# Performance work log

Measured on AMD Instinct MI355X. Metric: run time of the kernel, lower is better.

## Reference

```python
import jax, jax.numpy as jnp
import numpy as np

N_ORDER = 256
PRED_LEN = 192
SEQ_LEN = 768
ENC_IN = 21
BATCH = 16
MULTISCALE = [1, 2, 4]
MODES = 32  # min(32, min(pred_len, seq_len)//2)


def _transition(N):
    Q = np.arange(N, dtype=np.float64)
    R = (2 * Q + 1)[:, None]
    j, i = np.meshgrid(Q, Q)
    A = np.where(i < j, -1, (-1.0) ** (i - j + 1)) * R
    B = (-1.0) ** Q[:, None] * R
    return A, B


def _bilinear(A, B, dt):
    # scipy cont2discrete(method='bilinear'): Ad=(I-dt/2 A)^-1 (I+dt/2 A), Bd=(I-dt/2 A)^-1 dt B
    N = A.shape[0]
    I = np.eye(N)
    ima = I - (dt / 2.0) * A
    Ad = np.linalg.solve(ima, I + (dt / 2.0) * A)
    Bd = np.linalg.solve(ima, dt * B)
    return Ad, Bd.squeeze(-1)


def _legendre_eval(N, x):
    # Legendre P_n(x) via three-term recurrence; returns [len(x), N]
    T = x.shape[0]
    P = np.zeros((N, T))
    P[0] = 1.0
    if N > 1:
        P[1] = x
    for n in range(2, N):
        P[n] = ((2 * n - 1) * x * P[n - 1] - (n - 1) * P[n - 2]) / n
    return P.T


def setup_inputs() -> dict:
    key = jax.random.key(0)
    ks = jax.random.split(key, 12)
    inp = {"x_enc": jax.random.normal(ks[0], (BATCH, SEQ_LEN, ENC_IN), dtype=jnp.float32)}
    Ac, Bc = _transition(N_ORDER)
    scale = 1.0 / (N_ORDER * N_ORDER)
    for idx, m in enumerate(MULTISCALE):
        dt = 1.0 / PRED_LEN / m
        Ad, Bd = _bilinear(Ac, Bc, dt)
        vals = np.arange(0.0, 1.0, dt)
        E = _legendre_eval(N_ORDER, 1.0 - 2.0 * vals)
        inp[f"A{idx}"] = jnp.asarray(Ad, jnp.float32)
        inp[f"B{idx}"] = jnp.asarray(Bd, jnp.float32)
        inp[f"E{idx}"] = jnp.asarray(E, jnp.float32)
        inp[f"Wr{idx}"] = scale * jax.random.uniform(ks[1 + 2 * idx], (N_ORDER, N_ORDER, MODES), dtype=jnp.float32)
        inp[f"Wi{idx}"] = scale * jax.random.uniform(ks[2 + 2 * idx], (N_ORDER, N_ORDER, MODES), dtype=jnp.float32)
    inp["mlp_w"] = 0.1 * jax.random.normal(ks[10], (1, len(MULTISCALE)), dtype=jnp.float32)
    inp["mlp_b"] = jnp.zeros((1,), jnp.float32)
    return inp


def _hippo(x, A, Bv):
    # x: [B, E, L]; c_t = c_{t-1} @ A^T + f_t * B  (F.linear(c, A) == c @ A.T)
    def step(c, f):
        c = c @ A.T + f[..., None] * Bv
        return c, c
    c0 = jnp.zeros(x.shape[:-1] + (A.shape[0],), x.dtype)
    _, cs = jax.lax.scan(step, c0, jnp.moveaxis(x, -1, 0))
    return jnp.moveaxis(cs, 0, -1)  # [B, E, N, L]


def _spec_conv(x, Wr, Wi):
    # x: [B, E, N_in, L]; keep first MODES rfft modes, complex channel mix, irfft
    L = x.shape[-1]
    a = jnp.fft.rfft(x, axis=-1)[..., :MODES]
    W = (Wr + 1j * Wi).astype(jnp.complex64)
    out = jnp.einsum('bjix,iox->bjox', a, W)
    nf = L // 2 + 1
    out_full = jnp.pad(out, ((0, 0), (0, 0), (0, 0), (0, nf - MODES)))
    return jnp.fft.irfft(out_full, n=L, axis=-1)


def reference(x_enc, A0, B0, E0, Wr0, Wi0, A1, B1, E1, Wr1, Wi1, A2, B2, E2, Wr2, Wi2, mlp_w, mlp_b):
    params = [(A0, B0, E0, Wr0, Wi0), (A1, B1, E1, Wr1, Wi1), (A2, B2, E2, Wr2, Wi2)]
    x_decs = []
    for m, (A, Bv, E, Wr, Wi) in zip(MULTISCALE, params):
        x_in = x_enc[:, -m * PRED_LEN:]                      # [B, L, E]
        c = _hippo(jnp.transpose(x_in, (0, 2, 1)), A, Bv)    # [B, E, N, L]
        out1 = _spec_conv(c, Wr, Wi)                         # [B, E, N, L]
        x_dec_c = out1[:, :, :, PRED_LEN - 1]                # seq_len >= pred_len, jump_dist=0
        x_decs.append(x_dec_c @ E[-PRED_LEN:].T)             # [B, E, pred_len]
    x_dec = jnp.stack(x_decs, axis=-1)                       # [B, E, pred_len, 3]
    out = x_dec @ mlp_w[0] + mlp_b[0]                        # Linear(3,1) then squeeze
    return jnp.transpose(out, (0, 2, 1))                     # [B, pred_len, E]
```

## Files before the change

kernel.cpp:

```cpp
#include <hip/hip_runtime.h>
#include <math.h>

#define PI_F 3.14159265358979323846f

#define W_OFF    0
#define AP_OFF   344064
#define KT_OFF   737280
#define KTOT_OFF 995328
#define Y_OFF    1142784
#define S_OFF    1142784
#define F_OFF    1732608
#define QT_OFF   10579968
#define WS_FLOATS 27095040

__device__ __forceinline__ int off_w_f(int s)  { return 49152  * ((1 << s) - 1); }
__device__ __forceinline__ int qoff_f(int s)   { return 2359296 * ((1 << s) - 1); }
__device__ __forceinline__ int ktoff_f(int s)  { return 36864  * ((1 << s) - 1); }
__device__ __forceinline__ int foff_f(int s)   { return 1179648 * ((1 << s) - 1); }

template<bool BT>
__device__ __forceinline__ void gemm_tile(const float* __restrict__ A,
                                          const float* __restrict__ B,
                                          float* __restrict__ C,
                                          int M, int N, int ldc, int m0, int n0)
{
    __shared__ float As[16][68];
    __shared__ float Bs[16][68];
    const int tid = threadIdx.x;
    const int tx = tid & 15;
    const int ty = tid >> 4;
    const int r  = tid >> 2;
    const int kq = (tid & 3) << 2;

    float acc[4][4] = {{0.f,0.f,0.f,0.f},{0.f,0.f,0.f,0.f},
                       {0.f,0.f,0.f,0.f},{0.f,0.f,0.f,0.f}};

    for (int kk = 0; kk < 256; kk += 16) {
        float4 av = make_float4(0.f, 0.f, 0.f, 0.f);
        if (m0 + r < M)
            av = *(const float4*)(A + (size_t)(m0 + r) * 256 + kk + kq);
        As[kq + 0][r] = av.x; As[kq + 1][r] = av.y;
        As[kq + 2][r] = av.z; As[kq + 3][r] = av.w;

        if (BT) {
            float4 bv = make_float4(0.f, 0.f, 0.f, 0.f);
            if (n0 + r < N)
                bv = *(const float4*)(B + (size_t)(n0 + r) * 256 + kk + kq);
            Bs[kq + 0][r] = bv.x; Bs[kq + 1][r] = bv.y;
            Bs[kq + 2][r] = bv.z; Bs[kq + 3][r] = bv.w;
        } else {
            const int kb = tid >> 4;
            const int j4 = (tid & 15) << 2;
            float4 bv = *(const float4*)(B + (size_t)(kk + kb) * 256 + n0 + j4);
            *(float4*)(&Bs[kb][j4]) = bv;
        }
        __syncthreads();

        #pragma unroll
        for (int k = 0; k < 16; ++k) {
            float4 a4 = *(const float4*)(&As[k][ty << 2]);
            float4 b4 = *(const float4*)(&Bs[k][tx << 2]);
            acc[0][0] = fmaf(a4.x, b4.x, acc[0][0]);
            acc[0][1] = fmaf(a4.x, b4.y, acc[0][1]);
            acc[0][2] = fmaf(a4.x, b4.z, acc[0][2]);
            acc[0][3] = fmaf(a4.x, b4.w, acc[0][3]);
            acc[1][0] = fmaf(a4.y, b4.x, acc[1][0]);
            acc[1][1] = fmaf(a4.y, b4.y, acc[1][1]);
            acc[1][2] = fmaf(a4.y, b4.z, acc[1][2]);
            acc[1][3] = fmaf(a4.y, b4.w, acc[1][3]);
            acc[2][0] = fmaf(a4.z, b4.x, acc[2][0]);
            acc[2][1] = fmaf(a4.z, b4.y, acc[2][1]);
            acc[2][2] = fmaf(a4.z, b4.z, acc[2][2]);
            acc[2][3] = fmaf(a4.z, b4.w, acc[2][3]);
            acc[3][0] = fmaf(a4.w, b4.x, acc[3][0]);
            acc[3][1] = fmaf(a4.w, b4.y, acc[3][1]);
            acc[3][2] = fmaf(a4.w, b4.z, acc[3][2]);
            acc[3][3] = fmaf(a4.w, b4.w, acc[3][3]);
        }
        __syncthreads();
    }

    #pragma unroll
    for (int u = 0; u < 4; ++u) {
        int row = m0 + (ty << 2) + u;
        if (row < M) {
            float4 cv = make_float4(acc[u][0], acc[u][1], acc[u][2], acc[u][3]);
            *(float4*)(C + (size_t)row * ldc + n0 + (tx << 2)) = cv;
        }
    }
}

__device__ __forceinline__ void gemm64x128(const float* __restrict__ A,
                                           const float* __restrict__ B,
                                           float* __restrict__ C, int ldc)
{
    __shared__ float As[16][68];
    __shared__ float Bs[16][132];

    const int tid = threadIdx.x;
    const int tx = tid & 15;
    const int ty = tid >> 4;
    const int ra  = tid >> 2;
    const int kqa = (tid & 3) << 2;
    const int rb  = tid >> 1;
    const int kq8 = (tid & 1) << 3;

    float acc[2][4][4];
    #pragma unroll
    for (int g = 0; g < 2; ++g)
        #pragma unroll
        for (int u = 0; u < 4; ++u)
            #pragma unroll
            for (int v = 0; v < 4; ++v) acc[g][u][v] = 0.f;

    for (int kk = 0; kk < 256; kk += 16) {
        float4 av = *(const float4*)(A + (size_t)ra * 256 + kk + kqa);
        As[kqa + 0][ra] = av.x; As[kqa + 1][ra] = av.y;
        As[kqa + 2][ra] = av.z; As[kqa + 3][ra] = av.w;

        const float* bp = B + (size_t)rb * 256 + kk + kq8;
        float4 b0 = *(const float4*)(bp);
        float4 b1 = *(const float4*)(bp + 4);
        Bs[kq8 + 0][rb] = b0.x; Bs[kq8 + 1][rb] = b0.y;
        Bs[kq8 + 2][rb] = b0.z; Bs[kq8 + 3][rb] = b0.w;
        Bs[kq8 + 4][rb] = b1.x; Bs[kq8 + 5][rb] = b1.y;
        Bs[kq8 + 6][rb] = b1.z; Bs[kq8 + 7][rb] = b1.w;
        __syncthreads();

        #pragma unroll
        for (int kq = 0; kq < 16; ++kq) {
            float4 a  = *(const float4*)(&As[kq][4 * ty]);
            float4 b0v = *(const float4*)(&Bs[kq][4 * tx]);
            float4 b1v = *(const float4*)(&Bs[kq][4 * tx + 64]);
            float af[4] = {a.x, a.y, a.z, a.w};
            float bf[8] = {b0v.x, b0v.y, b0v.z, b0v.w, b1v.x, b1v.y, b1v.z, b1v.w};
            #pragma unroll
            for (int g = 0; g < 2; ++g)
                #pragma unroll
                for (int u = 0; u < 4; ++u)
                    #pragma unroll
                    for (int v = 0; v < 4; ++v)
                        acc[g][u][v] = fmaf(af[u], bf[g * 4 + v], acc[g][u][v]);
        }
        __syncthreads();
    }

    #pragma unroll
    for (int u = 0; u < 4; ++u) {
        int row = 4 * ty + u;
        #pragma unroll
        for (int g = 0; g < 2; ++g) {
            float4 cv = make_float4(acc[g][u][0], acc[g][u][1],
                                    acc[g][u][2], acc[g][u][3]);
            *(float4*)(C + (size_t)row * ldc + 4 * tx + 64 * g) = cv;
        }
    }
}

__global__ void k_init(const float* B0, const float* B1, const float* B2, float* ws)
{
    int s = blockIdx.x;
    const float* Bv = (s == 0) ? B0 : (s == 1) ? B1 : B2;
    ws[W_OFF + off_w_f(s) + threadIdx.x] = Bv[threadIdx.x];
}

__global__ void k_level(int n, const float* A0, const float* A1, const float* A2,
                        float* ws)
{
    int s = blockIdx.z;
    int L = 192 << s;
    const float* Ain = (s == 0) ? A0 : (s == 1) ? A1 : A2;
    float* wbase = ws + W_OFF + off_w_f(s);
    float* bufA  = ws + AP_OFF + s * 131072;
    float* bufB  = bufA + 65536;
    const float* src = (n == 0) ? Ain : (((n - 1) & 1) ? bufB : bufA);

    int y = blockIdx.y;
    if (y < 4) {
        int p2 = 1 << n;
        if (p2 >= L) return;
        int cnt = min(p2, L - p2);
        int m0 = y * 64;
        if (m0 >= cnt) return;
        gemm_tile<true>(wbase, src, wbase + (size_t)p2 * 256,
                        cnt, 256, 256, m0, blockIdx.x * 64);
    } else {
        if ((2 << n) >= L) return;
        float* dst = (n & 1) ? bufB : bufA;
        gemm_tile<false>(src, src, dst, 256, 256, 256, (y - 4) * 64, blockIdx.x * 64);
    }
}

__global__ void k_transpose(const float* Wr0, const float* Wi0,
                            const float* Wr1, const float* Wi1,
                            const float* Wr2, const float* Wi2, float* ws)
{
    int bid = blockIdx.x;
    int i  = bid & 255;
    int ri = (bid >> 8) & 1;
    int s  = bid >> 9;
    const float* W;
    if (s == 0)      W = ri ? Wi0 : Wr0;
    else if (s == 1) W = ri ? Wi1 : Wr1;
    else             W = ri ? Wi2 : Wr2;

    int o = threadIdx.x;
    int sri = s * 2 + ri;
    const float* Wrow = W + (size_t)i * 8192 + (size_t)o * 32;
    #pragma unroll
    for (int k = 0; k < 32; ++k) {
        ws[QT_OFF + ((size_t)(sri * 32 + k) * 256 + i) * 256 + o] = Wrow[k];
    }
}

__global__ void __launch_bounds__(256, 4)
k_gemm_Y4(const float* E0, const float* E1, const float* E2, float* __restrict__ ws)
{
    const int s  = blockIdx.z;
    const int L  = 192 << s;
    const int zz = blockIdx.x >> 1;
    const int n0 = (blockIdx.x & 1) * 128;
    const int z  = s * 64 + zz;
    const int m0 = blockIdx.y * 64;
    const float* E = (s == 0) ? E0 : (s == 1) ? E1 : E2;

    const float* Ap = E + (size_t)(L - 192) * 256 + (size_t)m0 * 256;
    const float* Bp = ws + QT_OFF + (size_t)z * 65536 + (size_t)n0 * 256;
    float* Cp = ws + Y_OFF + (size_t)z * 49152 + (size_t)m0 * 256 + n0;
    gemm64x128(Ap, Bp, Cp, 256);
}

__global__ void __launch_bounds__(256, 4)
k_gemm_Q4(float* __restrict__ ws)
{
    const int y = blockIdx.y;
    int s, yt;
    if (y < 3)      { s = 0; yt = y; }
    else if (y < 9) { s = 1; yt = y - 3; }
    else            { s = 2; yt = y - 9; }
    const int m0 = yt * 64;
    const int n0 = blockIdx.x * 128;

    const float* Ap = ws + W_OFF + off_w_f(s) + (size_t)m0 * 256;
    const float* Bp = ws + Y_OFF + (size_t)s * 3145728 + (size_t)n0 * 256;
    float* Cp = ws + QT_OFF + qoff_f(s) + (size_t)m0 * 12288 + n0;
    gemm64x128(Ap, Bp, Cp, 12288);
}

__global__ void k_scanA(float* __restrict__ ws)
{
    const int c = blockIdx.x;
    const int k = blockIdx.y;
    const int s = blockIdx.z;
    const int L = 192 << s;
    const int C = L >> 4;
    const int p = threadIdx.x;

    __shared__ float twc[768], tws[768];
    for (int m = p; m < L; m += 192) {
        float ang = -2.f * PI_F * (float)m / (float)L;
        float ss, cc; sincosf(ang, &ss, &cc);
        twc[m] = cc; tws[m] = ss;
    }
    __syncthreads();

    const float* Qr = ws + QT_OFF + qoff_f(s) + (size_t)k * 192;
    const float* Qi = Qr + 6144;

    float ar = 0.f, ai = 0.f;
    const int d0 = c * C;
    int ph = (k * d0) % L;
    for (int j = 0; j < C; ++j) {
        int d = d0 + j;
        float qr = Qr[(size_t)d * 12288 + p];
        float qi = Qi[(size_t)d * 12288 + p];
        float cc = twc[ph], sn = tws[ph];
        ar = fmaf(cc, qr, fmaf(-sn, qi, ar));
        ai = fmaf(cc, qi, fmaf( sn, qr, ai));
        ph += k; if (ph >= L) ph -= L;
    }
    size_t sb = (size_t)((s * 32 + k) * 16 + c) * 384;
    ws[S_OFF + sb + p]       = ar;
    ws[S_OFF + sb + 192 + p] = ai;
}

__global__ void k_scanB(float* __restrict__ ws)
{
    const int c = blockIdx.x;
    const int k = blockIdx.y;
    const int s = blockIdx.z;
    const int L = 192 << s;
    const int C = L >> 4;
    const int p = threadIdx.x;

    __shared__ float twc[768], tws[768];
    for (int m = p; m < L; m += 192) {
        float ang = -2.f * PI_F * (float)m / (float)L;
        float ss, cc; sincosf(ang, &ss, &cc);
        twc[m] = cc; tws[m] = ss;
    }
    __syncthreads();

    float ar = 0.f, ai = 0.f;
    size_t sbase = (size_t)(s * 32 + k) * 16 * 384;
    for (int c2 = 0; c2 < c; ++c2) {
        ar += ws[S_OFF + sbase + (size_t)c2 * 384 + p];
        ai += ws[S_OFF + sbase + (size_t)c2 * 384 + 192 + p];
    }

    const float ck = ((k == 0) ? 1.f : 2.f) / (float)L;
    const float* Qr = ws + QT_OFF + qoff_f(s) + (size_t)k * 192;
    const float* Qi = Qr + 6144;
    float* F = ws + F_OFF + foff_f(s);

    const int d0 = c * C;
    int ph = (k * d0) % L;
    int m1 = d0 + 192 - L; if (m1 < 0) m1 += L;
    int ph2 = (k * m1) % L;
    for (int j = 0; j < C; ++j) {
        int d = d0 + j;
        float qr = Qr[(size_t)d * 12288 + p];
        float qi = Qi[(size_t)d * 12288 + p];
        float cc = twc[ph], sn = tws[ph];
        ar = fmaf(cc, qr, fmaf(-sn, qi, ar));
        ai = fmaf(cc, qi, fmaf( sn, qr, ai));
        float f = ck * fmaf(twc[ph2], ar, tws[ph2] * ai);
        int sidx = L - 1 - d;
        F[((size_t)sidx * 32 + k) * 192 + p] = f;
        ph  += k; if (ph  >= L) ph  -= L;
        ph2 += k; if (ph2 >= L) ph2 -= L;
    }
}

__global__ void k_kred(float* __restrict__ ws)
{
    int bid = blockIdx.x;
    int s, sidx;
    if (bid < 192)      { s = 0; sidx = bid; }
    else if (bid < 576) { s = 1; sidx = bid - 192; }
    else                { s = 2; sidx = bid - 576; }
    int p = threadIdx.x;
    const float* F = ws + F_OFF + foff_f(s) + (size_t)sidx * 32 * 192;
    float sum = 0.f;
    #pragma unroll
    for (int k = 0; k < 32; ++k)
        sum += F[k * 192 + p];
    ws[KT_OFF + ktoff_f(s) + (size_t)sidx * 192 + p] = sum;
}

__global__ void k_combine(float* ws, const float* mw)
{
    int idx = blockIdx.x * 256 + threadIdx.x;
    if (idx >= 147456) return;
    int tau = idx / 192;
    int p   = idx - tau * 192;
    float sum = 0.f;
    #pragma unroll
    for (int s = 0; s < 3; ++s) {
        int L = 192 << s;
        int off = 768 - L;
        if (tau >= off)
            sum = fmaf(mw[s], ws[KT_OFF + ktoff_f(s) + (size_t)(tau - off) * 192 + p], sum);
    }
    ws[KTOT_OFF + idx] = sum;
}

__global__ void k_out(const float* __restrict__ x, const float* __restrict__ ws,
                      const float* __restrict__ mb, float* __restrict__ out)
{
    int bid = blockIdx.x;
    int b = bid / 21;
    int c = bid - b * 21;
    __shared__ float xl[768];
    for (int t = threadIdx.x; t < 768; t += 192)
        xl[t] = x[((size_t)b * 768 + t) * 21 + c];
    __syncthreads();

    int p = threadIdx.x;
    const float* K = ws + KTOT_OFF;
    float acc = 0.f;
    for (int tau = 0; tau < 768; ++tau)
        acc = fmaf(xl[tau], K[(size_t)tau * 192 + p], acc);
    out[((size_t)b * 192 + p) * 21 + c] = acc + mb[0];
}

extern "C" void kernel_launch(void* const* d_in, const int* in_sizes, int n_in,
                              void* d_out, int out_size, void* d_ws, size_t ws_size,
                              hipStream_t stream)
{
    const float* x   = (const float*)d_in[0];
    const float* A0  = (const float*)d_in[1];
    const float* B0  = (const float*)d_in[2];
    const float* E0  = (const float*)d_in[3];
    const float* Wr0 = (const float*)d_in[4];
    const float* Wi0 = (const float*)d_in[5];
    const float* A1  = (const float*)d_in[6];
    const float* B1  = (const float*)d_in[7];
    const float* E1  = (const float*)d_in[8];
    const float* Wr1 = (const float*)d_in[9];
    const float* Wi1 = (const float*)d_in[10];
    const float* A2  = (const float*)d_in[11];
    const float* B2  = (const float*)d_in[12];
    const float* E2  = (const float*)d_in[13];
    const float* Wr2 = (const float*)d_in[14];
    const float* Wi2 = (const float*)d_in[15];
    const float* mw  = (const float*)d_in[16];
    const float* mb  = (const float*)d_in[17];
    float* ws  = (float*)d_ws;
    float* out = (float*)d_out;

    if (ws_size < (size_t)WS_FLOATS * sizeof(float)) {
        hipMemsetAsync(d_out, 0, (size_t)out_size * sizeof(float), stream);
        return;
    }

    k_init<<<3, 256, 0, stream>>>(B0, B1, B2, ws);
    for (int n = 0; n < 10; ++n)
        k_level<<<dim3(4, 8, 3), 256, 0, stream>>>(n, A0, A1, A2, ws);
    k_transpose<<<1536, 256, 0, stream>>>(Wr0, Wi0, Wr1, Wi1, Wr2, Wi2, ws);
    k_gemm_Y4<<<dim3(128, 3, 3), 256, 0, stream>>>(E0, E1, E2, ws);
    k_gemm_Q4<<<dim3(96, 21), 256, 0, stream>>>(ws);
    k_scanA<<<dim3(16, 32, 3), 192, 0, stream>>>(ws);
    k_scanB<<<dim3(16, 32, 3), 192, 0, stream>>>(ws);
    k_kred<<<1344, 192, 0, stream>>>(ws);
    k_combine<<<576, 256, 0, stream>>>(ws, mw);
    k_out<<<336, 192, 0, stream>>>(x, ws, mb, out);
}
```

Measured before the change: 471.4 us.

## Coalesce weight transpose via LDS, fuse k-reduction with combine, trim level launches

```diff
diff --git a/kernel.cpp b/kernel.cpp
--- a/kernel.cpp
+++ b/kernel.cpp
@@ -15,7 +15,6 @@
 
 __device__ __forceinline__ int off_w_f(int s)  { return 49152  * ((1 << s) - 1); }
 __device__ __forceinline__ int qoff_f(int s)   { return 2359296 * ((1 << s) - 1); }
-__device__ __forceinline__ int ktoff_f(int s)  { return 36864  * ((1 << s) - 1); }
 __device__ __forceinline__ int foff_f(int s)   { return 1179648 * ((1 << s) - 1); }
 
 template<bool BT>
@@ -90,9 +89,9 @@
     }
 }
 
-__device__ __forceinline__ void gemm64x128(const float* __restrict__ A,
-                                           const float* __restrict__ B,
-                                           float* __restrict__ C, int ldc)
+__device__ __forceinline__ void gemm64x128_q(const float* __restrict__ A,
+                                             const float* __restrict__ B,
+                                             float* __restrict__ C, int ldc)
 {
     __shared__ float As[16][68];
     __shared__ float Bs[16][132];
@@ -129,7 +128,7 @@
 
         #pragma unroll
         for (int kq = 0; kq < 16; ++kq) {
-            float4 a  = *(const float4*)(&As[kq][4 * ty]);
+            float4 a   = *(const float4*)(&As[kq][4 * ty]);
             float4 b0v = *(const float4*)(&Bs[kq][4 * tx]);
             float4 b1v = *(const float4*)(&Bs[kq][4 * tx + 64]);
             float af[4] = {a.x, a.y, a.z, a.w};
@@ -164,10 +163,10 @@
     ws[W_OFF + off_w_f(s) + threadIdx.x] = Bv[threadIdx.x];
 }
 
-__global__ void k_level(int n, const float* A0, const float* A1, const float* A2,
-                        float* ws)
-{
-    int s = blockIdx.z;
+__global__ void k_level(int n, int sbase, const float* A0, const float* A1,
+                        const float* A2, float* ws)
+{
+    int s = blockIdx.z + sbase;
     int L = 192 << s;
     const float* Ain = (s == 0) ? A0 : (s == 1) ? A1 : A2;
     float* wbase = ws + W_OFF + off_w_f(s);
@@ -195,6 +194,7 @@
                             const float* Wr1, const float* Wi1,
                             const float* Wr2, const float* Wi2, float* ws)
 {
+    __shared__ float t[256][33];
     int bid = blockIdx.x;
     int i  = bid & 255;
     int ri = (bid >> 8) & 1;
@@ -204,30 +204,40 @@
     else if (s == 1) W = ri ? Wi1 : Wr1;
     else             W = ri ? Wi2 : Wr2;
 
-    int o = threadIdx.x;
+    const int tid = threadIdx.x;
+    const float* slab = W + (size_t)i * 8192;
+    #pragma unroll
+    for (int j = 0; j < 8; ++j) {
+        int f = j * 1024 + tid * 4;
+        float4 v = *(const float4*)(slab + f);
+        int o = f >> 5;
+        int k = f & 31;
+        t[o][k + 0] = v.x; t[o][k + 1] = v.y;
+        t[o][k + 2] = v.z; t[o][k + 3] = v.w;
+    }
+    __syncthreads();
+
     int sri = s * 2 + ri;
-    const float* Wrow = W + (size_t)i * 8192 + (size_t)o * 32;
     #pragma unroll
     for (int k = 0; k < 32; ++k) {
-        ws[QT_OFF + ((size_t)(sri * 32 + k) * 256 + i) * 256 + o] = Wrow[k];
+        ws[QT_OFF + (size_t)(sri * 32 + k) * 65536 + (size_t)i * 256 + tid] = t[tid][k];
     }
 }
 
 __global__ void __launch_bounds__(256, 4)
-k_gemm_Y4(const float* E0, const float* E1, const float* E2, float* __restrict__ ws)
-{
-    const int s  = blockIdx.z;
+k_gemm_Y5(const float* E0, const float* E1, const float* E2, float* __restrict__ ws)
+{
+    const int z  = blockIdx.z;
+    const int s  = z >> 6;
     const int L  = 192 << s;
-    const int zz = blockIdx.x >> 1;
-    const int n0 = (blockIdx.x & 1) * 128;
-    const int z  = s * 64 + zz;
+    const int n0 = blockIdx.x * 128;
     const int m0 = blockIdx.y * 64;
     const float* E = (s == 0) ? E0 : (s == 1) ? E1 : E2;
 
     const float* Ap = E + (size_t)(L - 192) * 256 + (size_t)m0 * 256;
     const float* Bp = ws + QT_OFF + (size_t)z * 65536 + (size_t)n0 * 256;
     float* Cp = ws + Y_OFF + (size_t)z * 49152 + (size_t)m0 * 256 + n0;
-    gemm64x128(Ap, Bp, Cp, 256);
+    gemm64x128_q(Ap, Bp, Cp, 256);
 }
 
 __global__ void __launch_bounds__(256, 4)
@@ -244,7 +254,7 @@
     const float* Ap = ws + W_OFF + off_w_f(s) + (size_t)m0 * 256;
     const float* Bp = ws + Y_OFF + (size_t)s * 3145728 + (size_t)n0 * 256;
     float* Cp = ws + QT_OFF + qoff_f(s) + (size_t)m0 * 12288 + n0;
-    gemm64x128(Ap, Bp, Cp, 12288);
+    gemm64x128_q(Ap, Bp, Cp, 12288);
 }
 
 __global__ void k_scanA(float* __restrict__ ws)
@@ -332,37 +342,26 @@
     }
 }
 
-__global__ void k_kred(float* __restrict__ ws)
-{
-    int bid = blockIdx.x;
-    int s, sidx;
-    if (bid < 192)      { s = 0; sidx = bid; }
-    else if (bid < 576) { s = 1; sidx = bid - 192; }
-    else                { s = 2; sidx = bid - 576; }
-    int p = threadIdx.x;
-    const float* F = ws + F_OFF + foff_f(s) + (size_t)sidx * 32 * 192;
-    float sum = 0.f;
-    #pragma unroll
-    for (int k = 0; k < 32; ++k)
-        sum += F[k * 192 + p];
-    ws[KT_OFF + ktoff_f(s) + (size_t)sidx * 192 + p] = sum;
-}
-
-__global__ void k_combine(float* ws, const float* mw)
-{
-    int idx = blockIdx.x * 256 + threadIdx.x;
-    if (idx >= 147456) return;
-    int tau = idx / 192;
-    int p   = idx - tau * 192;
+__global__ void k_kredc(float* __restrict__ ws, const float* __restrict__ mw)
+{
+    const int tau = blockIdx.x;
+    const int p   = threadIdx.x;
     float sum = 0.f;
     #pragma unroll
     for (int s = 0; s < 3; ++s) {
         int L = 192 << s;
         int off = 768 - L;
-        if (tau >= off)
-            sum = fmaf(mw[s], ws[KT_OFF + ktoff_f(s) + (size_t)(tau - off) * 192 + p], sum);
-    }
-    ws[KTOT_OFF + idx] = sum;
+        if (tau >= off) {
+            int sidx = tau - off;
+            const float* F = ws + F_OFF + foff_f(s) + (size_t)sidx * 32 * 192;
+            float kt = 0.f;
+            #pragma unroll
+            for (int k = 0; k < 32; ++k)
+                kt += F[k * 192 + p];
+            sum = fmaf(mw[s], kt, sum);
+        }
+    }
+    ws[KTOT_OFF + (size_t)tau * 192 + p] = sum;
 }
 
 __global__ void k_out(const float* __restrict__ x, const float* __restrict__ ws,
@@ -415,14 +414,15 @@
     }
 
     k_init<<<3, 256, 0, stream>>>(B0, B1, B2, ws);
-    for (int n = 0; n < 10; ++n)
-        k_level<<<dim3(4, 8, 3), 256, 0, stream>>>(n, A0, A1, A2, ws);
+    for (int n = 0; n < 8; ++n)
+        k_level<<<dim3(4, 8, 3), 256, 0, stream>>>(n, 0, A0, A1, A2, ws);
+    k_level<<<dim3(4, 8, 2), 256, 0, stream>>>(8, 1, A0, A1, A2, ws);
+    k_level<<<dim3(4, 8, 1), 256, 0, stream>>>(9, 2, A0, A1, A2, ws);
     k_transpose<<<1536, 256, 0, stream>>>(Wr0, Wi0, Wr1, Wi1, Wr2, Wi2, ws);
-    k_gemm_Y4<<<dim3(128, 3, 3), 256, 0, stream>>>(E0, E1, E2, ws);
+    k_gemm_Y5<<<dim3(2, 3, 192), 256, 0, stream>>>(E0, E1, E2, ws);
     k_gemm_Q4<<<dim3(96, 21), 256, 0, stream>>>(ws);
     k_scanA<<<dim3(16, 32, 3), 192, 0, stream>>>(ws);
     k_scanB<<<dim3(16, 32, 3), 192, 0, stream>>>(ws);
-    k_kred<<<1344, 192, 0, stream>>>(ws);
-    k_combine<<<576, 256, 0, stream>>>(ws, mw);
+    k_kredc<<<768, 192, 0, stream>>>(ws, mw);
     k_out<<<336, 192, 0, stream>>>(x, ws, mb, out);
 }
```

New measurement: 421.7 us. 10.5% less time.
